# Kernel optimization log

Hardware: AMD Instinct MI355X
Metric: run time of the kernel (lower is better)

The kernel has to match this reference:

```python
import jax, jax.numpy as jnp
import numpy as np

N, C, L, E, H = 2000, 4, 5000, 64000, 512
REP = 207  # length after conv front-end: floor((floor((5000-11)/4)+1 - 11)/6)+1


def setup_inputs() -> dict:
    key = jax.random.key(0)
    ks = jax.random.split(key, 10)

    def init(k, shape, fan_in):
        return jax.random.normal(k, shape, jnp.float32) / np.sqrt(fan_in).astype(np.float32)

    x = jax.random.normal(ks[0], (N, C, L), jnp.float32)
    edge_index = jax.random.randint(ks[1], (2, E), 0, N)
    return dict(
        x=x, edge_index=edge_index,
        w1=init(ks[2], (16, C, 1), C), b1=jnp.zeros(16, jnp.float32),
        w2=init(ks[3], (4, 4, 11), 4 * 11), b2=jnp.zeros(4, jnp.float32),
        w3=init(ks[4], (1, 4, 11), 4 * 11), b3=jnp.zeros(1, jnp.float32),
        gcn_w=init(ks[5], (REP, H), REP), gcn_b=jnp.zeros(H, jnp.float32),
        lin_w=init(ks[6], (REP, H), REP), lin_b=jnp.zeros(H, jnp.float32),
        gate_w=init(ks[7], (H, H), H), gate_b=jnp.zeros(H, jnp.float32),
        bn_gamma=jnp.ones(H, jnp.float32), bn_beta=jnp.zeros(H, jnp.float32),
    )


def _conv1d(x, w, b, stride):
    # x: [N, Cin, L], w: [Cout, Cin, K] (torch OIH layout), VALID padding
    y = jax.lax.conv_general_dilated(x, w, (stride,), 'VALID',
                                     dimension_numbers=('NCH', 'OIH', 'NCH'))
    return y + b[None, :, None]


def _gcn_conv(feat, edge_index, w, b, n):
    # GCNConv: x@W, add self-loops, sym-normalize, scatter-add, + bias
    h = feat @ w                                      # [N, H]
    loops = jnp.arange(n)
    src = jnp.concatenate([edge_index[0], loops])
    dst = jnp.concatenate([edge_index[1], loops])
    deg = jax.ops.segment_sum(jnp.ones_like(src, h.dtype), dst, num_segments=n)
    dinv = jax.lax.rsqrt(deg)                         # deg >= 1 due to self-loops
    norm = dinv[src] * dinv[dst]                      # [E+N]
    out = jax.ops.segment_sum(h[src] * norm[:, None], dst, num_segments=n)
    return out + b


def reference(x, edge_index, w1, b1, w2, b2, w3, b3,
              gcn_w, gcn_b, lin_w, lin_b, gate_w, gate_b, bn_gamma, bn_beta):
    n = x.shape[0]
    # conv front-end (dropout layers are identity at inference)
    h = jax.nn.relu(_conv1d(x, w1, b1, 1))            # [N, 16, L]
    # MaxPool1d(k=4,s=4) applied on permuted [N, L, 16] == pool over channel dim
    h = h.reshape(n, 4, 4, L).max(axis=2)             # [N, 4, L]
    h = jax.nn.relu(_conv1d(h, w2, b2, 4))            # [N, 4, 1248]
    h = jax.nn.relu(_conv1d(h, w3, b3, 6))            # [N, 1, 207]
    feat = h[:, 0, :]                                 # squeeze -> [N, REP]
    # GCN + gated fusion
    z = jnp.tanh(_gcn_conv(feat, edge_index, gcn_w, gcn_b, n))
    g = jax.nn.sigmoid(z @ gate_w + gate_b)
    xl = feat @ lin_w + lin_b
    out = jax.nn.relu((1.0 - g) * xl + g * z)
    # BatchNorm over node dim (batch statistics, training-mode semantics)
    mean = out.mean(axis=0)
    var = out.var(axis=0)
    out = (out - mean) * jax.lax.rsqrt(var + 1e-5) * bn_gamma + bn_beta
    return out
```

## Files before the change

### kernel.cpp

```cpp
#include <hip/hip_runtime.h>
#include <hip/hip_bf16.h>
#include <cstddef>

#define NN 2000
#define CC 4
#define LL1 5000
#define LL2 1248
#define LL3 207
#define HH 512
#define EE 64000

__device__ __forceinline__ float bf2f_lo(unsigned int u) { return __uint_as_float(u << 16); }
__device__ __forceinline__ float bf2f_hi(unsigned int u) { return __uint_as_float(u & 0xffff0000u); }
__device__ __forceinline__ unsigned int f2bf(float v) {
    __hip_bfloat16 h = __float2bfloat16(v);
    unsigned short u; __builtin_memcpy(&u, &h, 2);
    return (unsigned int)u;
}

__device__ float g_feat[NN * LL3];
__device__ float g_aggf[NN * LL3];
__device__ float g_z[NN * HH];
__device__ float g_xl[NN * HH];
__device__ float g_gpre[NN * HH];
__device__ float g_obuf[NN * HH];
__device__ float g_dinv[NN];
__device__ float g_colsum[HH];
__device__ float g_colsq[HH];
__device__ float g_sc[HH];
__device__ float g_sh[HH];
__device__ int   g_cnt[NN];
__device__ int   g_cursor[NN];
__device__ int   g_off[NN];
__device__ int   g_bucket[EE];

__global__ void zero_init() {
    int i = blockIdx.x * 256 + threadIdx.x;
    if (i < NN) { g_cnt[i] = 0; g_cursor[i] = 0; }
    if (i < HH) { g_colsum[i] = 0.f; g_colsq[i] = 0.f; }
}

#define HB_DW 1256
#define HB_U2 628
__global__ __launch_bounds__(256) void conv_chain(
    const float* __restrict__ x,
    const float* __restrict__ w1, const float* __restrict__ b1,
    const float* __restrict__ w2, const float* __restrict__ b2,
    const float* __restrict__ w3, const float* __restrict__ b3)
{
    __shared__ __align__(16) unsigned int smu[4 * HB_DW];
    __shared__ float sy[4 * LL2];

    const int tid = threadIdx.x;
    const int node = blockIdx.x;
    const float* xb = x + (size_t)node * (CC * LL1);

    float w1r[64], b1r[16];
#pragma unroll
    for (int i = 0; i < 64; ++i) w1r[i] = w1[i];
#pragma unroll
    for (int i = 0; i < 16; ++i) b1r[i] = b1[i];

    uint2* smu2 = (uint2*)smu;

    for (int h = 0; h < 2; ++h) {
        const int l0 = h * 2496;
        for (int g4 = tid; g4 < 626; g4 += 256) {
            const int l = l0 + 4 * g4;
            float xs[4][4];
#pragma unroll
            for (int c = 0; c < 4; ++c)
                *(float4*)xs[c] = *(const float4*)(xb + c * LL1 + l);
#pragma unroll
            for (int g = 0; g < 4; ++g) {
                float mv[4];
#pragma unroll
                for (int li = 0; li < 4; ++li) {
                    float best = -1e30f;
#pragma unroll
                    for (int j = 0; j < 4; ++j) {
                        int o = g * 4 + j;
                        float v = b1r[o] + w1r[o*4+0]*xs[0][li] + w1r[o*4+1]*xs[1][li]
                                         + w1r[o*4+2]*xs[2][li] + w1r[o*4+3]*xs[3][li];
                        best = fmaxf(best, v);
                    }
                    mv[li] = fmaxf(best, 0.f);
                }
                uint2 p;
                p.x = f2bf(mv[0]) | (f2bf(mv[1]) << 16);
                p.y = f2bf(mv[2]) | (f2bf(mv[3]) << 16);
                smu2[g * HB_U2 + g4] = p;
            }
        }
        __syncthreads();

        const int T0 = h * 624;
        for (int t = T0 + tid; t < T0 + 624; t += 256) {
            const int T = t - T0;
            float acc0 = b2[0], acc1 = b2[1], acc2 = b2[2], acc3 = b2[3];
#pragma unroll
            for (int i = 0; i < 4; ++i) {
                const int ub = i * HB_U2 + T;
                uint2 r0 = smu2[ub], r1 = smu2[ub + 1], r2 = smu2[ub + 2];
                float v[12];
                v[0] = bf2f_lo(r0.x); v[1] = bf2f_hi(r0.x);
                v[2] = bf2f_lo(r0.y); v[3] = bf2f_hi(r0.y);
                v[4] = bf2f_lo(r1.x); v[5] = bf2f_hi(r1.x);
                v[6] = bf2f_lo(r1.y); v[7] = bf2f_hi(r1.y);
                v[8] = bf2f_lo(r2.x); v[9] = bf2f_hi(r2.x);
                v[10] = bf2f_lo(r2.y); v[11] = bf2f_hi(r2.y);
#pragma unroll
                for (int k = 0; k < 11; ++k) {
                    float vv = v[k];
                    acc0 += w2[0*44 + i*11 + k] * vv;
                    acc1 += w2[1*44 + i*11 + k] * vv;
                    acc2 += w2[2*44 + i*11 + k] * vv;
                    acc3 += w2[3*44 + i*11 + k] * vv;
                }
            }
            sy[0 * LL2 + t] = fmaxf(acc0, 0.f);
            sy[1 * LL2 + t] = fmaxf(acc1, 0.f);
            sy[2 * LL2 + t] = fmaxf(acc2, 0.f);
            sy[3 * LL2 + t] = fmaxf(acc3, 0.f);
        }
        __syncthreads();
    }

    if (tid < LL3) {
        float acc = b3[0];
#pragma unroll
        for (int i = 0; i < 4; ++i)
#pragma unroll
            for (int k = 0; k < 11; ++k)
                acc += w3[i * 11 + k] * sy[i * LL2 + 6 * tid + k];
        g_feat[(size_t)node * LL3 + tid] = fmaxf(acc, 0.f);
    }
}

__global__ void edge_count(const int* __restrict__ ei, int E) {
    int e = blockIdx.x * 256 + threadIdx.x;
    if (e < E) atomicAdd(&g_cnt[ei[E + e]], 1);
}

__global__ __launch_bounds__(256) void scan_dinv() {
    __shared__ int a[2048], b[2048];
    int tid = threadIdx.x;
    for (int i = tid; i < 2048; i += 256) a[i] = (i < NN) ? g_cnt[i] : 0;
    __syncthreads();
    int* src = a; int* dst = b;
    for (int d = 1; d < 2048; d <<= 1) {
        for (int i = tid; i < 2048; i += 256)
            dst[i] = src[i] + ((i >= d) ? src[i - d] : 0);
        __syncthreads();
        int* t = src; src = dst; dst = t;
    }
    for (int i = tid; i < NN; i += 256) {
        g_off[i] = src[i] - g_cnt[i];
        g_dinv[i] = rsqrtf(1.0f + (float)g_cnt[i]);
    }
}

__global__ void bucket_fill(const int* __restrict__ ei, int E) {
    int e = blockIdx.x * 256 + threadIdx.x;
    if (e < E) {
        int d = ei[E + e];
        int p = atomicAdd(&g_cursor[d], 1);
        g_bucket[g_off[d] + p] = ei[e];
    }
}

__global__ __launch_bounds__(256) void agg_feat() {
    const int d = blockIdx.x;
    const int tid = threadIdx.x;
    if (tid >= LL3) return;
    const float di = g_dinv[d];
    const int nb = g_cnt[d];
    const int base = g_off[d];
    float acc = g_feat[(size_t)d * LL3 + tid] * di;
    int j = 0;
    for (; j + 1 < nb; j += 2) {
        int s0 = g_bucket[base + j];
        int s1 = g_bucket[base + j + 1];
        acc += g_feat[(size_t)s0 * LL3 + tid] * g_dinv[s0]
             + g_feat[(size_t)s1 * LL3 + tid] * g_dinv[s1];
    }
    if (j < nb) {
        int s = g_bucket[base + j];
        acc += g_feat[(size_t)s * LL3 + tid] * g_dinv[s];
    }
    g_aggf[(size_t)d * LL3 + tid] = acc * di;
}

template<int EPI>
__global__ __launch_bounds__(256) void gemm32(
    const float* __restrict__ A, const float* __restrict__ B,
    const float* __restrict__ bias, float* __restrict__ C,
    int M, int N, int K)
{
    __shared__ float As[2][16][32];
    __shared__ float Bs[2][16][64];
    const int tid = threadIdx.x;
    const int N0 = blockIdx.x * 64, M0 = blockIdx.y * 32;
    const int tx = tid & 15, ty = tid >> 4;
    const int ar = tid >> 3, ak = (tid & 7) * 2;
    const int bk = tid >> 4, bn = (tid & 15) * 4;
    const int NT = (K + 15) / 16;

    float acc[2][4] = {};
    float a0, a1; float4 b4r;

    {
        int r = M0 + ar;
        a0 = (r < M && ak < K) ? A[(size_t)r * K + ak] : 0.f;
        a1 = (r < M && ak + 1 < K) ? A[(size_t)r * K + ak + 1] : 0.f;
        b4r = (bk < K) ? *(const float4*)(B + (size_t)bk * N + N0 + bn) : make_float4(0,0,0,0);
        As[0][ak][ar] = a0; As[0][ak + 1][ar] = a1;
        *(float4*)&Bs[0][bk][bn] = b4r;
    }
    __syncthreads();

    for (int kt = 0; kt < NT; ++kt) {
        const int cur = kt & 1;
        if (kt + 1 < NT) {
            int k0 = (kt + 1) * 16;
            int r = M0 + ar;
            int kk = k0 + ak;
            a0 = (r < M && kk < K) ? A[(size_t)r * K + kk] : 0.f;
            a1 = (r < M && kk + 1 < K) ? A[(size_t)r * K + kk + 1] : 0.f;
            int kb = k0 + bk;
            b4r = (kb < K) ? *(const float4*)(B + (size_t)kb * N + N0 + bn) : make_float4(0,0,0,0);
        }
#pragma unroll
        for (int k = 0; k < 16; ++k) {
            float2 a2 = *(const float2*)&As[cur][k][ty * 2];
            float4 b4 = *(const float4*)&Bs[cur][k][tx * 4];
            acc[0][0] += a2.x * b4.x; acc[0][1] += a2.x * b4.y;
            acc[0][2] += a2.x * b4.z; acc[0][3] += a2.x * b4.w;
            acc[1][0] += a2.y * b4.x; acc[1][1] += a2.y * b4.y;
            acc[1][2] += a2.y * b4.z; acc[1][3] += a2.y * b4.w;
        }
        if (kt + 1 < NT) {
            const int nxt = cur ^ 1;
            As[nxt][ak][ar] = a0; As[nxt][ak + 1][ar] = a1;
            *(float4*)&Bs[nxt][bk][bn] = b4r;
        }
        __syncthreads();
    }

    float bb[4];
#pragma unroll
    for (int j = 0; j < 4; ++j) bb[j] = bias ? bias[N0 + tx * 4 + j] : 0.f;
#pragma unroll
    for (int i = 0; i < 2; ++i) {
        int r = M0 + ty * 2 + i;
        if (r < M) {
#pragma unroll
            for (int j = 0; j < 4; ++j) {
                float v = acc[i][j] + bb[j];
                if (EPI == 1) v = tanhf(v);
                C[(size_t)r * N + N0 + tx * 4 + j] = v;
            }
        }
    }
}

__global__ __launch_bounds__(256) void gate_bn() {
    const int tid = threadIdx.x;
    const int r0 = blockIdx.x * 8;
    float a0 = 0, a1 = 0, q0 = 0, q1 = 0;
    for (int r = r0; r < r0 + 8; ++r) {
        size_t i0 = (size_t)r * HH + tid;
        size_t i1 = i0 + 256;
        float g0 = 1.f / (1.f + expf(-g_gpre[i0]));
        float g1 = 1.f / (1.f + expf(-g_gpre[i1]));
        float v0 = fmaxf((1.f - g0) * g_xl[i0] + g0 * g_z[i0], 0.f);
        float v1 = fmaxf((1.f - g1) * g_xl[i1] + g1 * g_z[i1], 0.f);
        g_obuf[i0] = v0; g_obuf[i1] = v1;
        a0 += v0; q0 += v0 * v0;
        a1 += v1; q1 += v1 * v1;
    }
    atomicAdd(&g_colsum[tid], a0);
    atomicAdd(&g_colsum[tid + 256], a1);
    atomicAdd(&g_colsq[tid], q0);
    atomicAdd(&g_colsq[tid + 256], q1);
}

__global__ void bn_stats(const float* __restrict__ gamma, const float* __restrict__ beta) {
    int c = threadIdx.x;
    float mean = g_colsum[c] * (1.f / (float)NN);
    float var = g_colsq[c] * (1.f / (float)NN) - mean * mean;
    float s = rsqrtf(var + 1e-5f) * gamma[c];
    g_sc[c] = s;
    g_sh[c] = beta[c] - mean * s;
}

__global__ __launch_bounds__(256) void bn_apply(float* __restrict__ out) {
    int i = blockIdx.x * 256 + threadIdx.x;
    int c = i & (HH - 1);
    out[i] = g_obuf[i] * g_sc[c] + g_sh[c];
}

extern "C" void kernel_launch(void* const* d_in, const int* in_sizes, int n_in,
                              void* d_out, int out_size, void* d_ws, size_t ws_size,
                              hipStream_t stream) {
    (void)d_ws; (void)ws_size; (void)n_in; (void)out_size;
    const float* x      = (const float*)d_in[0];
    const int*   ei     = (const int*)d_in[1];
    const float* w1     = (const float*)d_in[2];
    const float* b1     = (const float*)d_in[3];
    const float* w2     = (const float*)d_in[4];
    const float* b2     = (const float*)d_in[5];
    const float* w3     = (const float*)d_in[6];
    const float* b3     = (const float*)d_in[7];
    const float* gcn_w  = (const float*)d_in[8];
    const float* gcn_b  = (const float*)d_in[9];
    const float* lin_w  = (const float*)d_in[10];
    const float* lin_b  = (const float*)d_in[11];
    const float* gate_w = (const float*)d_in[12];
    const float* gate_b = (const float*)d_in[13];
    const float* bn_g   = (const float*)d_in[14];
    const float* bn_b   = (const float*)d_in[15];
    float* out = (float*)d_out;
    const int E = in_sizes[1] / 2;

    float* feat = nullptr; float* aggf = nullptr; float* z = nullptr;
    float* xl = nullptr; float* gpre = nullptr;
    hipGetSymbolAddress((void**)&feat, HIP_SYMBOL(g_feat));
    hipGetSymbolAddress((void**)&aggf, HIP_SYMBOL(g_aggf));
    hipGetSymbolAddress((void**)&z,    HIP_SYMBOL(g_z));
    hipGetSymbolAddress((void**)&xl,   HIP_SYMBOL(g_xl));
    hipGetSymbolAddress((void**)&gpre, HIP_SYMBOL(g_gpre));

    zero_init<<<8, 256, 0, stream>>>();
    conv_chain<<<NN, 256, 0, stream>>>(x, w1, b1, w2, b2, w3, b3);
    edge_count<<<(E + 255) / 256, 256, 0, stream>>>(ei, E);
    scan_dinv<<<1, 256, 0, stream>>>();
    bucket_fill<<<(E + 255) / 256, 256, 0, stream>>>(ei, E);
    agg_feat<<<NN, 256, 0, stream>>>();

    dim3 gg(HH / 64, (NN + 31) / 32);
    gemm32<1><<<gg, 256, 0, stream>>>(aggf, gcn_w, gcn_b, z, NN, HH, LL3);
    gemm32<0><<<gg, 256, 0, stream>>>(feat, lin_w, lin_b, xl, NN, HH, LL3);
    gemm32<0><<<gg, 256, 0, stream>>>(z, gate_w, gate_b, gpre, NN, HH, HH);

    gate_bn<<<NN / 8, 256, 0, stream>>>();
    bn_stats<<<1, HH, 0, stream>>>(bn_g, bn_b);
    bn_apply<<<(NN * HH) / 256, 256, 0, stream>>>(out);
}
```

Before: 406.4 us.

## Use fp32 shared conv staging, 64x64 GEMM tiles, and fuse gating/BN stats into GEMM

Measured after the change: 386.1 us. 5.0% less time.

```diff
diff --git a/kernel.cpp b/kernel.cpp
--- a/kernel.cpp
+++ b/kernel.cpp
@@ -10,19 +10,10 @@
 #define HH 512
 #define EE 64000
 
-__device__ __forceinline__ float bf2f_lo(unsigned int u) { return __uint_as_float(u << 16); }
-__device__ __forceinline__ float bf2f_hi(unsigned int u) { return __uint_as_float(u & 0xffff0000u); }
-__device__ __forceinline__ unsigned int f2bf(float v) {
-    __hip_bfloat16 h = __float2bfloat16(v);
-    unsigned short u; __builtin_memcpy(&u, &h, 2);
-    return (unsigned int)u;
-}
-
 __device__ float g_feat[NN * LL3];
 __device__ float g_aggf[NN * LL3];
 __device__ float g_z[NN * HH];
 __device__ float g_xl[NN * HH];
-__device__ float g_gpre[NN * HH];
 __device__ float g_obuf[NN * HH];
 __device__ float g_dinv[NN];
 __device__ float g_colsum[HH];
@@ -40,16 +31,15 @@
     if (i < HH) { g_colsum[i] = 0.f; g_colsq[i] = 0.f; }
 }
 
-#define HB_DW 1256
-#define HB_U2 628
+#define MCH 1256
 __global__ __launch_bounds__(256) void conv_chain(
     const float* __restrict__ x,
     const float* __restrict__ w1, const float* __restrict__ b1,
     const float* __restrict__ w2, const float* __restrict__ b2,
     const float* __restrict__ w3, const float* __restrict__ b3)
 {
-    __shared__ __align__(16) unsigned int smu[4 * HB_DW];
-    __shared__ float sy[4 * LL2];
+    __shared__ __align__(16) float sm[4 * MCH];
+    __shared__ __align__(16) float sy[4 * LL2];
 
     const int tid = threadIdx.x;
     const int node = blockIdx.x;
@@ -61,16 +51,15 @@
 #pragma unroll
     for (int i = 0; i < 16; ++i) b1r[i] = b1[i];
 
-    uint2* smu2 = (uint2*)smu;
-
-    for (int h = 0; h < 2; ++h) {
-        const int l0 = h * 2496;
-        for (int g4 = tid; g4 < 626; g4 += 256) {
+#pragma unroll 1
+    for (int c = 0; c < 4; ++c) {
+        const int l0 = 1248 * c;
+        for (int g4 = tid; g4 < 314; g4 += 256) {
             const int l = l0 + 4 * g4;
             float xs[4][4];
 #pragma unroll
-            for (int c = 0; c < 4; ++c)
-                *(float4*)xs[c] = *(const float4*)(xb + c * LL1 + l);
+            for (int ch = 0; ch < 4; ++ch)
+                *(float4*)xs[ch] = *(const float4*)(xb + ch * LL1 + l);
 #pragma unroll
             for (int g = 0; g < 4; ++g) {
                 float mv[4];
@@ -86,42 +75,39 @@
                     }
                     mv[li] = fmaxf(best, 0.f);
                 }
-                uint2 p;
-                p.x = f2bf(mv[0]) | (f2bf(mv[1]) << 16);
-                p.y = f2bf(mv[2]) | (f2bf(mv[3]) << 16);
-                smu2[g * HB_U2 + g4] = p;
-            }
-        }
-        __syncthreads();
-
-        const int T0 = h * 624;
-        for (int t = T0 + tid; t < T0 + 624; t += 256) {
-            const int T = t - T0;
-            float acc0 = b2[0], acc1 = b2[1], acc2 = b2[2], acc3 = b2[3];
-#pragma unroll
-            for (int i = 0; i < 4; ++i) {
-                const int ub = i * HB_U2 + T;
-                uint2 r0 = smu2[ub], r1 = smu2[ub + 1], r2 = smu2[ub + 2];
-                float v[12];
-                v[0] = bf2f_lo(r0.x); v[1] = bf2f_hi(r0.x);
-                v[2] = bf2f_lo(r0.y); v[3] = bf2f_hi(r0.y);
-                v[4] = bf2f_lo(r1.x); v[5] = bf2f_hi(r1.x);
-                v[6] = bf2f_lo(r1.y); v[7] = bf2f_hi(r1.y);
-                v[8] = bf2f_lo(r2.x); v[9] = bf2f_hi(r2.x);
-                v[10] = bf2f_lo(r2.y); v[11] = bf2f_hi(r2.y);
-#pragma unroll
-                for (int k = 0; k < 11; ++k) {
-                    float vv = v[k];
-                    acc0 += w2[0*44 + i*11 + k] * vv;
-                    acc1 += w2[1*44 + i*11 + k] * vv;
-                    acc2 += w2[2*44 + i*11 + k] * vv;
-                    acc3 += w2[3*44 + i*11 + k] * vv;
+                *(float4*)&sm[g * MCH + 4 * g4] = make_float4(mv[0], mv[1], mv[2], mv[3]);
+            }
+        }
+        __syncthreads();
+
+        const int T0 = 312 * c;
+#pragma unroll 1
+        for (int pair = 0; pair < 2; ++pair) {
+            const float* wp = w2 + 88 * pair;
+            float wo[88];
+#pragma unroll
+            for (int i = 0; i < 88; ++i) wo[i] = wp[i];
+            const float bo0 = b2[2 * pair], bo1 = b2[2 * pair + 1];
+            for (int T = tid; T < 312; T += 256) {
+                float a0 = bo0, a1 = bo1;
+#pragma unroll
+                for (int i = 0; i < 4; ++i) {
+                    const float* mp = sm + i * MCH + 4 * T;
+                    float4 u0 = *(const float4*)mp;
+                    float4 u1 = *(const float4*)(mp + 4);
+                    float4 u2 = *(const float4*)(mp + 8);
+                    float v[12] = {u0.x, u0.y, u0.z, u0.w,
+                                   u1.x, u1.y, u1.z, u1.w,
+                                   u2.x, u2.y, u2.z, u2.w};
+#pragma unroll
+                    for (int k = 0; k < 11; ++k) {
+                        a0 += wo[i * 11 + k] * v[k];
+                        a1 += wo[44 + i * 11 + k] * v[k];
+                    }
                 }
-            }
-            sy[0 * LL2 + t] = fmaxf(acc0, 0.f);
-            sy[1 * LL2 + t] = fmaxf(acc1, 0.f);
-            sy[2 * LL2 + t] = fmaxf(acc2, 0.f);
-            sy[3 * LL2 + t] = fmaxf(acc3, 0.f);
+                sy[(2 * pair) * LL2 + T0 + T]     = fmaxf(a0, 0.f);
+                sy[(2 * pair + 1) * LL2 + T0 + T] = fmaxf(a1, 0.f);
+            }
         }
         __syncthreads();
     }
@@ -192,97 +178,123 @@
 }
 
 template<int EPI>
-__global__ __launch_bounds__(256) void gemm32(
+__global__ __launch_bounds__(256) void gemm64(
     const float* __restrict__ A, const float* __restrict__ B,
     const float* __restrict__ bias, float* __restrict__ C,
+    const float* __restrict__ xl, const float* __restrict__ zb,
     int M, int N, int K)
 {
-    __shared__ float As[2][16][32];
+    __shared__ float As[2][16][64];
     __shared__ float Bs[2][16][64];
+    __shared__ float rs[64], rq[64];
     const int tid = threadIdx.x;
-    const int N0 = blockIdx.x * 64, M0 = blockIdx.y * 32;
+    const int N0 = blockIdx.x * 64, M0 = blockIdx.y * 64;
     const int tx = tid & 15, ty = tid >> 4;
-    const int ar = tid >> 3, ak = (tid & 7) * 2;
+    const int ar = tid & 63, ac = (tid >> 6) * 4;
     const int bk = tid >> 4, bn = (tid & 15) * 4;
     const int NT = (K + 15) / 16;
 
-    float acc[2][4] = {};
-    float a0, a1; float4 b4r;
+    float acc[4][4] = {};
+    float ra[4]; float4 rb;
 
     {
         int r = M0 + ar;
-        a0 = (r < M && ak < K) ? A[(size_t)r * K + ak] : 0.f;
-        a1 = (r < M && ak + 1 < K) ? A[(size_t)r * K + ak + 1] : 0.f;
-        b4r = (bk < K) ? *(const float4*)(B + (size_t)bk * N + N0 + bn) : make_float4(0,0,0,0);
-        As[0][ak][ar] = a0; As[0][ak + 1][ar] = a1;
-        *(float4*)&Bs[0][bk][bn] = b4r;
+#pragma unroll
+        for (int q = 0; q < 4; ++q) {
+            int kk = ac + q;
+            ra[q] = (r < M && kk < K) ? A[(size_t)r * K + kk] : 0.f;
+        }
+        rb = (bk < K) ? *(const float4*)(B + (size_t)bk * N + N0 + bn) : make_float4(0,0,0,0);
+#pragma unroll
+        for (int q = 0; q < 4; ++q) As[0][ac + q][ar] = ra[q];
+        *(float4*)&Bs[0][bk][bn] = rb;
     }
     __syncthreads();
 
+#pragma unroll 1
     for (int kt = 0; kt < NT; ++kt) {
         const int cur = kt & 1;
         if (kt + 1 < NT) {
             int k0 = (kt + 1) * 16;
             int r = M0 + ar;
-            int kk = k0 + ak;
-            a0 = (r < M && kk < K) ? A[(size_t)r * K + kk] : 0.f;
-            a1 = (r < M && kk + 1 < K) ? A[(size_t)r * K + kk + 1] : 0.f;
+#pragma unroll
+            for (int q = 0; q < 4; ++q) {
+                int kk = k0 + ac + q;
+                ra[q] = (r < M && kk < K) ? A[(size_t)r * K + kk] : 0.f;
+            }
             int kb = k0 + bk;
-            b4r = (kb < K) ? *(const float4*)(B + (size_t)kb * N + N0 + bn) : make_float4(0,0,0,0);
+            rb = (kb < K) ? *(const float4*)(B + (size_t)kb * N + N0 + bn) : make_float4(0,0,0,0);
         }
 #pragma unroll
         for (int k = 0; k < 16; ++k) {
-            float2 a2 = *(const float2*)&As[cur][k][ty * 2];
+            float4 a4 = *(const float4*)&As[cur][k][ty * 4];
             float4 b4 = *(const float4*)&Bs[cur][k][tx * 4];
-            acc[0][0] += a2.x * b4.x; acc[0][1] += a2.x * b4.y;
-            acc[0][2] += a2.x * b4.z; acc[0][3] += a2.x * b4.w;
-            acc[1][0] += a2.y * b4.x; acc[1][1] += a2.y * b4.y;
-            acc[1][2] += a2.y * b4.z; acc[1][3] += a2.y * b4.w;
+            acc[0][0] += a4.x * b4.x; acc[0][1] += a4.x * b4.y; acc[0][2] += a4.x * b4.z; acc[0][3] += a4.x * b4.w;
+            acc[1][0] += a4.y * b4.x; acc[1][1] += a4.y * b4.y; acc[1][2] += a4.y * b4.z; acc[1][3] += a4.y * b4.w;
+            acc[2][0] += a4.z * b4.x; acc[2][1] += a4.z * b4.y; acc[2][2] += a4.z * b4.z; acc[2][3] += a4.z * b4.w;
+            acc[3][0] += a4.w * b4.x; acc[3][1] += a4.w * b4.y; acc[3][2] += a4.w * b4.z; acc[3][3] += a4.w * b4.w;
         }
         if (kt + 1 < NT) {
             const int nxt = cur ^ 1;
-            As[nxt][ak][ar] = a0; As[nxt][ak + 1][ar] = a1;
-            *(float4*)&Bs[nxt][bk][bn] = b4r;
-        }
-        __syncthreads();
-    }
-
-    float bb[4];
-#pragma unroll
-    for (int j = 0; j < 4; ++j) bb[j] = bias ? bias[N0 + tx * 4 + j] : 0.f;
-#pragma unroll
-    for (int i = 0; i < 2; ++i) {
-        int r = M0 + ty * 2 + i;
-        if (r < M) {
-#pragma unroll
-            for (int j = 0; j < 4; ++j) {
-                float v = acc[i][j] + bb[j];
-                if (EPI == 1) v = tanhf(v);
-                C[(size_t)r * N + N0 + tx * 4 + j] = v;
-            }
-        }
-    }
-}
-
-__global__ __launch_bounds__(256) void gate_bn() {
-    const int tid = threadIdx.x;
-    const int r0 = blockIdx.x * 8;
-    float a0 = 0, a1 = 0, q0 = 0, q1 = 0;
-    for (int r = r0; r < r0 + 8; ++r) {
-        size_t i0 = (size_t)r * HH + tid;
-        size_t i1 = i0 + 256;
-        float g0 = 1.f / (1.f + expf(-g_gpre[i0]));
-        float g1 = 1.f / (1.f + expf(-g_gpre[i1]));
-        float v0 = fmaxf((1.f - g0) * g_xl[i0] + g0 * g_z[i0], 0.f);
-        float v1 = fmaxf((1.f - g1) * g_xl[i1] + g1 * g_z[i1], 0.f);
-        g_obuf[i0] = v0; g_obuf[i1] = v1;
-        a0 += v0; q0 += v0 * v0;
-        a1 += v1; q1 += v1 * v1;
-    }
-    atomicAdd(&g_colsum[tid], a0);
-    atomicAdd(&g_colsum[tid + 256], a1);
-    atomicAdd(&g_colsq[tid], q0);
-    atomicAdd(&g_colsq[tid + 256], q1);
+#pragma unroll
+            for (int q = 0; q < 4; ++q) As[nxt][ac + q][ar] = ra[q];
+            *(float4*)&Bs[nxt][bk][bn] = rb;
+        }
+        __syncthreads();
+    }
+
+    const int c0 = N0 + tx * 4;
+    float4 bb4 = bias ? *(const float4*)(bias + c0) : make_float4(0,0,0,0);
+    float bb[4] = {bb4.x, bb4.y, bb4.z, bb4.w};
+
+    if (EPI == 2) {
+        float cs[4] = {0,0,0,0}, cq[4] = {0,0,0,0};
+#pragma unroll
+        for (int i = 0; i < 4; ++i) {
+            int r = M0 + ty * 4 + i;
+            if (r < M) {
+                float4 xv = *(const float4*)(xl + (size_t)r * N + c0);
+                float4 zv = *(const float4*)(zb + (size_t)r * N + c0);
+                float xa[4] = {xv.x, xv.y, xv.z, xv.w};
+                float za[4] = {zv.x, zv.y, zv.z, zv.w};
+                float va[4];
+#pragma unroll
+                for (int j = 0; j < 4; ++j) {
+                    float g = 1.f / (1.f + __expf(-(acc[i][j] + bb[j])));
+                    float v = fmaxf((1.f - g) * xa[j] + g * za[j], 0.f);
+                    va[j] = v; cs[j] += v; cq[j] += v * v;
+                }
+                *(float4*)(C + (size_t)r * N + c0) = make_float4(va[0], va[1], va[2], va[3]);
+            }
+        }
+        if (tid < 64) { rs[tid] = 0.f; rq[tid] = 0.f; }
+        __syncthreads();
+#pragma unroll
+        for (int j = 0; j < 4; ++j) {
+            atomicAdd(&rs[tx * 4 + j], cs[j]);
+            atomicAdd(&rq[tx * 4 + j], cq[j]);
+        }
+        __syncthreads();
+        if (tid < 64) {
+            atomicAdd(&g_colsum[N0 + tid], rs[tid]);
+            atomicAdd(&g_colsq[N0 + tid], rq[tid]);
+        }
+    } else {
+#pragma unroll
+        for (int i = 0; i < 4; ++i) {
+            int r = M0 + ty * 4 + i;
+            if (r < M) {
+                float va[4];
+#pragma unroll
+                for (int j = 0; j < 4; ++j) {
+                    float v = acc[i][j] + bb[j];
+                    if (EPI == 1) v = tanhf(v);
+                    va[j] = v;
+                }
+                *(float4*)(C + (size_t)r * N + c0) = make_float4(va[0], va[1], va[2], va[3]);
+            }
+        }
+    }
 }
 
 __global__ void bn_stats(const float* __restrict__ gamma, const float* __restrict__ beta) {
@@ -324,12 +336,12 @@
     const int E = in_sizes[1] / 2;
 
     float* feat = nullptr; float* aggf = nullptr; float* z = nullptr;
-    float* xl = nullptr; float* gpre = nullptr;
+    float* xl = nullptr; float* obuf = nullptr;
     hipGetSymbolAddress((void**)&feat, HIP_SYMBOL(g_feat));
     hipGetSymbolAddress((void**)&aggf, HIP_SYMBOL(g_aggf));
     hipGetSymbolAddress((void**)&z,    HIP_SYMBOL(g_z));
     hipGetSymbolAddress((void**)&xl,   HIP_SYMBOL(g_xl));
-    hipGetSymbolAddress((void**)&gpre, HIP_SYMBOL(g_gpre));
+    hipGetSymbolAddress((void**)&obuf, HIP_SYMBOL(g_obuf));
 
     zero_init<<<8, 256, 0, stream>>>();
     conv_chain<<<NN, 256, 0, stream>>>(x, w1, b1, w2, b2, w3, b3);
@@ -338,12 +350,11 @@
     bucket_fill<<<(E + 255) / 256, 256, 0, stream>>>(ei, E);
     agg_feat<<<NN, 256, 0, stream>>>();
 
-    dim3 gg(HH / 64, (NN + 31) / 32);
-    gemm32<1><<<gg, 256, 0, stream>>>(aggf, gcn_w, gcn_b, z, NN, HH, LL3);
-    gemm32<0><<<gg, 256, 0, stream>>>(feat, lin_w, lin_b, xl, NN, HH, LL3);
-    gemm32<0><<<gg, 256, 0, stream>>>(z, gate_w, gate_b, gpre, NN, HH, HH);
-
-    gate_bn<<<NN / 8, 256, 0, stream>>>();
+    dim3 gg(HH / 64, (NN + 63) / 64);
+    gemm64<1><<<gg, 256, 0, stream>>>(aggf, gcn_w, gcn_b, z, nullptr, nullptr, NN, HH, LL3);
+    gemm64<0><<<gg, 256, 0, stream>>>(feat, lin_w, lin_b, xl, nullptr, nullptr, NN, HH, LL3);
+    gemm64<2><<<gg, 256, 0, stream>>>(z, gate_w, gate_b, obuf, xl, z, NN, HH, HH);
+
     bn_stats<<<1, HH, 0, stream>>>(bn_g, bn_b);
     bn_apply<<<(NN * HH) / 256, 256, 0, stream>>>(out);
 }
```
